# Performance work log

Hardware: AMD Instinct MI355X
Metric: run time of the kernel (lower is better)

Reference implementation:

```python
import jax, jax.numpy as jnp
import numpy as np

B, E, F = 16384, 128, 6
ITEM_V, CATE_V, HIST = 91718, 11, 50
I_IDX, J_IDX = np.triu_indices(F, k=1)  # 15 field pairs, loop order (0,1),(0,2),...
EPS = 1e-5


def _xavier(key, shape):
    fan_in, fan_out = shape[0], shape[-1]
    std = (2.0 / (fan_in + fan_out)) ** 0.5
    return std * jax.random.normal(key, shape, dtype=jnp.float32)


def setup_inputs() -> dict:
    key = jax.random.key(0)
    ks = jax.random.split(key, 20)
    inp = {
        'item_id': jax.random.randint(ks[0], (B,), 0, ITEM_V),
        'item_emb_d128': jax.random.normal(ks[1], (B, 128), dtype=jnp.float32),
        'likes_level': jax.random.randint(ks[2], (B,), 0, CATE_V),
        'views_level': jax.random.randint(ks[3], (B,), 0, CATE_V),
        'item_seq': jax.random.randint(ks[4], (B, HIST), 0, ITEM_V),
        # learned parameters
        'item_emb': 0.05 * jax.random.normal(ks[5], (ITEM_V, E), dtype=jnp.float32),
        'cate_emb': 0.05 * jax.random.normal(ks[6], (CATE_V, E), dtype=jnp.float32),
        'mm_W': _xavier(ks[7], (128, E)), 'mm_b': jnp.zeros((E,), jnp.float32),
        'ln_g': jnp.ones((E,), jnp.float32), 'ln_b': jnp.zeros((E,), jnp.float32),
        'se_W1': _xavier(ks[8], (F, F // 2)), 'se_b1': jnp.zeros((F // 2,), jnp.float32),
        'se_W2': _xavier(ks[9], (F // 2, F)), 'se_b2': jnp.zeros((F,), jnp.float32),
        'bi_W': _xavier(ks[10], (E, E)),
        'mlp_W1': _xavier(ks[11], (21 * E, 512)), 'mlp_b1': jnp.zeros((512,), jnp.float32),
        'bn1_g': jnp.ones((512,), jnp.float32), 'bn1_b': jnp.zeros((512,), jnp.float32),
        'bn1_rm': jnp.zeros((512,), jnp.float32), 'bn1_rv': jnp.ones((512,), jnp.float32),
        'mlp_W2': _xavier(ks[12], (512, 256)), 'mlp_b2': jnp.zeros((256,), jnp.float32),
        'bn2_g': jnp.ones((256,), jnp.float32), 'bn2_b': jnp.zeros((256,), jnp.float32),
        'bn2_rm': jnp.zeros((256,), jnp.float32), 'bn2_rv': jnp.ones((256,), jnp.float32),
        'mlp_W3': _xavier(ks[13], (256, 1)), 'mlp_b3': jnp.zeros((1,), jnp.float32),
    }
    return inp


def _forward(item_id, item_emb_d128, likes_level, views_level, item_seq,
             item_emb, cate_emb, mm_W, mm_b, ln_g, ln_b,
             se_W1, se_b1, se_W2, se_b2, bi_W,
             mlp_W1, mlp_b1, bn1_g, bn1_b, bn1_rm, bn1_rv,
             mlp_W2, mlp_b2, bn2_g, bn2_b, bn2_rm, bn2_rv,
             mlp_W3, mlp_b3):
    b = item_id.shape[0]
    tab = item_emb.at[0].set(0.0)  # padding_idx=0
    like_feat = cate_emb[likes_level]
    view_feat = cate_emb[views_level]
    item_feat = tab[item_id]
    # mm_proj: Linear -> LayerNorm -> ReLU
    mm = item_emb_d128 @ mm_W + mm_b
    mu = mm.mean(-1, keepdims=True)
    var = jnp.var(mm, axis=-1, keepdims=True)
    mm = jax.nn.relu((mm - mu) / jnp.sqrt(var + EPS) * ln_g + ln_b)
    # masked mean pooling over history
    seq_emb = tab[item_seq]                               # (B, HIST, E)
    valid = (item_seq != 0).astype(seq_emb.dtype)
    seq_sum = (seq_emb * valid[..., None]).sum(1)
    cnt = jnp.clip(valid.sum(1, keepdims=True), 1.0)
    hist_feat = seq_sum / cnt
    user_feat = jnp.zeros((b, E), seq_emb.dtype)
    x = jnp.stack([user_feat, like_feat, view_feat, item_feat, mm, hist_feat], axis=1)  # (B,6,E)
    # SENet
    z = x.mean(-1)
    w = jax.nn.sigmoid(jax.nn.relu(z @ se_W1 + se_b1) @ se_W2 + se_b2)
    xs = x * w[:, :, None]
    # bilinear 'all'
    xw = jnp.einsum('bfe,ed->bfd', xs, bi_W)
    p = xs[:, I_IDX, :] * xw[:, J_IDX, :]                 # (B,15,E)
    c = jnp.concatenate([xs.reshape(b, -1), p.reshape(b, -1)], axis=1)  # (B, 2688)
    # MLP head (eval mode: BN uses running stats, dropout off)
    h = c @ mlp_W1 + mlp_b1
    h = jax.nn.relu((h - bn1_rm) / jnp.sqrt(bn1_rv + EPS) * bn1_g + bn1_b)
    h = h @ mlp_W2 + mlp_b2
    h = jax.nn.relu((h - bn2_rm) / jnp.sqrt(bn2_rv + EPS) * bn2_g + bn2_b)
    logits = h @ mlp_W3 + mlp_b3
    return jax.nn.sigmoid(logits)[:, 0]


def reference(item_id, item_emb_d128, likes_level, views_level, item_seq,
              item_emb, cate_emb, mm_W, mm_b, ln_g, ln_b,
              se_W1, se_b1, se_W2, se_b2, bi_W,
              mlp_W1, mlp_b1, bn1_g, bn1_b, bn1_rm, bn1_rv,
              mlp_W2, mlp_b2, bn2_g, bn2_b, bn2_rm, bn2_rv,
              mlp_W3, mlp_b3):
    return _forward(item_id, item_emb_d128, likes_level, views_level, item_seq,
                    item_emb, cate_emb, mm_W, mm_b, ln_g, ln_b,
                    se_W1, se_b1, se_W2, se_b2, bi_W,
                    mlp_W1, mlp_b1, bn1_g, bn1_b, bn1_rm, bn1_rv,
                    mlp_W2, mlp_b2, bn2_g, bn2_b, bn2_rm, bn2_rv,
                    mlp_W3, mlp_b3)
```

## Files before the change

### kernel.cpp

```cpp
#include <hip/hip_runtime.h>
#include <hip/hip_bf16.h>

typedef __hip_bfloat16 bfloat;
typedef __bf16 bf16x8 __attribute__((ext_vector_type(8)));
typedef float f32x4 __attribute__((ext_vector_type(4)));

#define B_SZ   16384
#define E_DIM  128
#define HIST_L 50


#define IPACK 0x3221110000ULL
#define JPACK 0x3323213210ULL

__device__ __forceinline__ void gl_lds16(const void* g, void* l) {
    __builtin_amdgcn_global_load_lds(
        (const __attribute__((address_space(1))) unsigned int*)g,
        (__attribute__((address_space(3))) unsigned int*)l, 16, 0, 0);
}

__device__ __forceinline__ bf16x8 mul_bf16x8(bf16x8 a, bf16x8 b) {
    union { bf16x8 v; __hip_bfloat162 h[4]; } ua, ub, ur;
    ua.v = a; ub.v = b;
    #pragma unroll
    for (int i = 0; i < 4; ++i) ur.h[i] = __hmul2(ua.h[i], ub.h[i]);
    return ur.v;
}

template<int TB>
__global__ __launch_bounds__(256) void feat_kernel(
    const int* __restrict__ item_id,
    const int* __restrict__ likes, const int* __restrict__ views,
    const int* __restrict__ seq,
    const void* __restrict__ item_tab, const float* __restrict__ cate_emb,
    const float* __restrict__ mm,
    const float* __restrict__ ln_g, const float* __restrict__ ln_b,
    const float* __restrict__ se_W1, const float* __restrict__ se_b1,
    const float* __restrict__ se_W2, const float* __restrict__ se_b2,
    bfloat* __restrict__ xs)
{
    const int tid = threadIdx.x;
    const int r   = tid >> 7;
    const int e   = tid & 127;
    const int b   = blockIdx.x * 2 + r;
    const int w   = tid >> 6;

    __shared__ float redh[2][4][128];
    __shared__ int   seq_s[2][64];
    __shared__ float lnred[4], lnred2[4];
    __shared__ float zred[5][4];
    __shared__ float wsh[2][6];
    __shared__ int   cnt_s[2];

    if (e < 64) seq_s[r][e] = (e < HIST_L) ? seq[(size_t)b * HIST_L + e] : 0;
    __syncthreads();

    const int iid = item_id[b];
    const float like_v = cate_emb[likes[b] * 128 + e];
    const float view_v = cate_emb[views[b] * 128 + e];
    float item_v;
    if (TB) {
        const bfloat* tb = (const bfloat*)item_tab;
        item_v = __bfloat162float(tb[(size_t)iid * 128 + e]);
    } else {
        const float* tf = (const float*)item_tab;
        float raw = tf[(size_t)iid * 128 + e];
        item_v = iid ? raw : 0.f;
    }
    const float acc = mm[(size_t)b * 128 + e];

    const int q   = e >> 5;
    const int l32 = e & 31;
    float4 hs = make_float4(0.f, 0.f, 0.f, 0.f);
    if (TB) {
        const ushort* tb = (const ushort*)item_tab;
        #pragma unroll
        for (int g = 0; g < 13; ++g) {
            int s = seq_s[r][g * 4 + q];
            ushort4 v = *(const ushort4*)&tb[(size_t)s * 128 + l32 * 4];
            hs.x += __bfloat162float(__ushort_as_bfloat16(v.x));
            hs.y += __bfloat162float(__ushort_as_bfloat16(v.y));
            hs.z += __bfloat162float(__ushort_as_bfloat16(v.z));
            hs.w += __bfloat162float(__ushort_as_bfloat16(v.w));
        }
    } else {
        const float* tf = (const float*)item_tab;
        #pragma unroll
        for (int g = 0; g < 13; ++g) {
            int s = seq_s[r][g * 4 + q];
            const float4 v = *(const float4*)&tf[(size_t)s * 128 + l32 * 4];
            float m = (s != 0) ? 1.f : 0.f;
            hs.x = fmaf(v.x, m, hs.x);
            hs.y = fmaf(v.y, m, hs.y);
            hs.z = fmaf(v.z, m, hs.z);
            hs.w = fmaf(v.w, m, hs.w);
        }
    }

    {
        float v = acc;
        #pragma unroll
        for (int off = 32; off > 0; off >>= 1) v += __shfl_down(v, off, 64);
        if ((tid & 63) == 0) lnred[w] = v;
    }
    __syncthreads();
    const float mu = (lnred[2 * r] + lnred[2 * r + 1]) * (1.f / 128.f);
    const float d  = acc - mu;
    {
        float v = d * d;
        #pragma unroll
        for (int off = 32; off > 0; off >>= 1) v += __shfl_down(v, off, 64);
        if ((tid & 63) == 0) lnred2[w] = v;
    }
    redh[r][q][l32 * 4 + 0] = hs.x;
    redh[r][q][l32 * 4 + 1] = hs.y;
    redh[r][q][l32 * 4 + 2] = hs.z;
    redh[r][q][l32 * 4 + 3] = hs.w;
    if ((w & 1) == 0 && e < 64) {
        bool valid = (e < HIST_L) && (seq_s[r][e] != 0);
        unsigned long long m = __ballot(valid);
        if (e == 0) cnt_s[r] = (int)__popcll(m);
    }
    __syncthreads();
    const float var = (lnred2[2 * r] + lnred2[2 * r + 1]) * (1.f / 128.f);
    float xmm = d * rsqrtf(var + 1e-5f) * ln_g[e] + ln_b[e];
    xmm = fmaxf(xmm, 0.f);

    const int cnt = cnt_s[r] > 0 ? cnt_s[r] : 1;
    const float hist_v = (redh[r][0][e] + redh[r][1][e] +
                          redh[r][2][e] + redh[r][3][e]) / (float)cnt;

    {
        float s1 = like_v, s2 = view_v, s3 = item_v, s4 = xmm, s5 = hist_v;
        #pragma unroll
        for (int off = 32; off > 0; off >>= 1) {
            s1 += __shfl_down(s1, off, 64);
            s2 += __shfl_down(s2, off, 64);
            s3 += __shfl_down(s3, off, 64);
            s4 += __shfl_down(s4, off, 64);
            s5 += __shfl_down(s5, off, 64);
        }
        if ((tid & 63) == 0) {
            zred[0][w] = s1; zred[1][w] = s2; zred[2][w] = s3;
            zred[3][w] = s4; zred[4][w] = s5;
        }
    }
    __syncthreads();

    if (e == 0) {
        float z[6];
        z[0] = 0.f;
        #pragma unroll
        for (int f = 1; f < 6; ++f)
            z[f] = (zred[f - 1][2 * r] + zred[f - 1][2 * r + 1]) * (1.f / 128.f);
        float a[3];
        #pragma unroll
        for (int j = 0; j < 3; ++j) {
            float s = se_b1[j];
            #pragma unroll
            for (int f = 0; f < 6; ++f) s += z[f] * se_W1[f * 3 + j];
            a[j] = fmaxf(s, 0.f);
        }
        #pragma unroll
        for (int f = 0; f < 6; ++f) {
            float s = se_b2[f];
            #pragma unroll
            for (int j = 0; j < 3; ++j) s += a[j] * se_W2[j * 6 + f];
            wsh[r][f] = 1.f / (1.f + expf(-s));
        }
    }
    __syncthreads();

    bfloat* xrow = xs + (size_t)b * 640;
    xrow[0 * 128 + e] = __float2bfloat16(like_v * wsh[r][1]);
    xrow[1 * 128 + e] = __float2bfloat16(view_v * wsh[r][2]);
    xrow[2 * 128 + e] = __float2bfloat16(item_v * wsh[r][3]);
    xrow[3 * 128 + e] = __float2bfloat16(xmm    * wsh[r][4]);
    xrow[4 * 128 + e] = __float2bfloat16(hist_v * wsh[r][5]);
}

__global__ __launch_bounds__(256) void transpose_W1c(
    const float* __restrict__ W1, bfloat* __restrict__ W1t)
{
    int idx = blockIdx.x * 256 + threadIdx.x;
    if (idx < 512 * 1920) {
        int n = idx / 1920, kk = idx % 1920;
        int orig = kk + (kk < 640 ? 128 : 768);
        W1t[idx] = __float2bfloat16(W1[(size_t)orig * 512 + n]);
    }
}

__global__ __launch_bounds__(256) void prep_kernel(
    const float* __restrict__ W2, const float* __restrict__ bi_W,
    const float* __restrict__ mm_W,
    bfloat* __restrict__ W2t, bfloat* __restrict__ bWt,
    bfloat* __restrict__ mmWt,
    const float* __restrict__ lb1, const float* __restrict__ g1,
    const float* __restrict__ bb1, const float* __restrict__ rm1,
    const float* __restrict__ rv1,
    const float* __restrict__ lb2, const float* __restrict__ g2,
    const float* __restrict__ bb2, const float* __restrict__ rm2,
    const float* __restrict__ rv2,
    const float* __restrict__ mm_b,
    float* __restrict__ S1, float* __restrict__ T1,
    float* __restrict__ S2, float* __restrict__ T2,
    float* __restrict__ Tmm)
{
    int idx = blockIdx.x * 256 + threadIdx.x;
    if (idx < 131072) {
        int k = idx >> 8, n = idx & 255;
        W2t[(size_t)n * 512 + k] = __float2bfloat16(W2[idx]);
    } else if (idx < 147456) {
        int t = idx - 131072;
        int k = t >> 7, n = t & 127;
        bWt[n * 128 + k] = __float2bfloat16(bi_W[t]);
    } else if (idx < 163840) {
        int t = idx - 147456;
        int k = t >> 7, n = t & 127;
        mmWt[n * 128 + k] = __float2bfloat16(mm_W[t]);
    } else if (idx < 164352) {
        int j = idx - 163840;
        float s = g1[j] * rsqrtf(rv1[j] + 1e-5f);
        S1[j] = s;
        T1[j] = (lb1[j] - rm1[j]) * s + bb1[j];
    } else if (idx < 164608) {
        int j = idx - 164352;
        float s = g2[j] * rsqrtf(rv2[j] + 1e-5f);
        S2[j] = s;
        T2[j] = (lb2[j] - rm2[j]) * s + bb2[j];
    } else if (idx < 164736) {
        int j = idx - 164608;
        Tmm[j] = mm_b[j];
    }
}

__global__ __launch_bounds__(256) void cvt_emb(
    const float* __restrict__ in, bfloat* __restrict__ out, int n8)
{
    int idx = blockIdx.x * 256 + threadIdx.x;
    if (idx >= n8) return;
    if (idx < 16) {
        union { bf16x8 v; unsigned short s[8]; } z;
        #pragma unroll
        for (int i = 0; i < 8; ++i) z.s[i] = 0;
        ((bf16x8*)out)[idx] = z.v;
        return;
    }
    float4 f0 = ((const float4*)in)[idx * 2];
    float4 f1 = ((const float4*)in)[idx * 2 + 1];
    union { bf16x8 v; unsigned short s[8]; } u;
    u.s[0] = __bfloat16_as_ushort(__float2bfloat16(f0.x));
    u.s[1] = __bfloat16_as_ushort(__float2bfloat16(f0.y));
    u.s[2] = __bfloat16_as_ushort(__float2bfloat16(f0.z));
    u.s[3] = __bfloat16_as_ushort(__float2bfloat16(f0.w));
    u.s[4] = __bfloat16_as_ushort(__float2bfloat16(f1.x));
    u.s[5] = __bfloat16_as_ushort(__float2bfloat16(f1.y));
    u.s[6] = __bfloat16_as_ushort(__float2bfloat16(f1.z));
    u.s[7] = __bfloat16_as_ushort(__float2bfloat16(f1.w));
    ((bf16x8*)out)[idx] = u.v;
}

__global__ __launch_bounds__(256) void pair_kernel(
    const bfloat* __restrict__ xs, const bfloat* __restrict__ xw,
    bfloat* __restrict__ P, int total)
{
    int idx = blockIdx.x * 256 + threadIdx.x;
    if (idx >= total) return;
    int b = idx / 160, c = idx % 160;
    int pp = c >> 4, q = c & 15;
    int isl = (int)((IPACK >> (4 * pp)) & 15);
    int jsl = (int)((JPACK >> (4 * pp)) & 15);
    bf16x8 a = *(const bf16x8*)&xs[(size_t)b * 640 + isl * 128 + q * 8];
    bf16x8 w = *(const bf16x8*)&xw[((size_t)b * 4 + jsl) * 128 + q * 8];
    *(bf16x8*)&P[(size_t)b * 1280 + c * 8] = mul_bf16x8(a, w);
}

template<int MODE, int EPI, int F32OUT>
__global__ __launch_bounds__(256) void gemm_bt(
    const void* __restrict__ A, const bfloat* __restrict__ A2,
    const bfloat* __restrict__ Bt, void* __restrict__ C,
    int M, int N, int K,
    const float* __restrict__ S, const float* __restrict__ T)
{
    __shared__ __align__(16) short As[3][64 * 64];
    __shared__ __align__(16) short Bs[3][64 * 64];

    const int tid  = threadIdx.x;
    const int bm   = blockIdx.x * 64;
    const int bn   = blockIdx.y * 64;
    const int wave = tid >> 6;
    const int lane = tid & 63;
    const int wm   = (wave >> 1) * 32;
    const int wn   = (wave & 1) * 32;

    const short* Ag  = (const short*)A;
    const short* A2g = (const short*)A2;
    const short* Bg  = (const short*)Bt;

    f32x4 acc[2][2];
    #pragma unroll
    for (int i = 0; i < 2; ++i)
        #pragma unroll
        for (int j = 0; j < 2; ++j)
            acc[i][j] = (f32x4){0.f, 0.f, 0.f, 0.f};

    const int srow = tid >> 3;
    const int sck  = tid & 7;

    auto stage = [&](int buf, int kt) {
        #pragma unroll
        for (int rr = 0; rr < 2; ++rr) {
            int row = srow + rr * 32;
            int g   = sck ^ (row & 7);
            gl_lds16(&Bg[(long)(bn + row) * K + kt + g * 8],
                     &Bs[buf][row * 64 + sck * 8]);
        }
        if (MODE == 3) {
            const float* Af = (const float*)A;
            #pragma unroll
            for (int rr = 0; rr < 2; ++rr) {
                int row = srow + rr * 32;
                int g   = sck ^ (row & 7);
                long aoff = (long)(bm + row) * K + kt + g * 8;
                float4 f0 = *(const float4*)&Af[aoff];
                float4 f1 = *(const float4*)&Af[aoff + 4];
                union { bf16x8 v; unsigned short s[8]; } u;
                u.s[0] = __bfloat16_as_ushort(__float2bfloat16(f0.x));
                u.s[1] = __bfloat16_as_ushort(__float2bfloat16(f0.y));
                u.s[2] = __bfloat16_as_ushort(__float2bfloat16(f0.z));
                u.s[3] = __bfloat16_as_ushort(__float2bfloat16(f0.w));
                u.s[4] = __bfloat16_as_ushort(__float2bfloat16(f1.x));
                u.s[5] = __bfloat16_as_ushort(__float2bfloat16(f1.y));
                u.s[6] = __bfloat16_as_ushort(__float2bfloat16(f1.z));
                u.s[7] = __bfloat16_as_ushort(__float2bfloat16(f1.w));
                *(bf16x8*)&As[buf][row * 64 + sck * 8] = u.v;
            }
        } else {
            #pragma unroll
            for (int rr = 0; rr < 2; ++rr) {
                int row = srow + rr * 32;
                int g   = sck ^ (row & 7);
                const short* src;
                if (MODE == 4) {
                    long rb = (long)(bm + row);
                    src = (kt < 640)
                        ? &Ag [rb * 640  + kt + g * 8]
                        : &A2g[rb * 1280 + (kt - 640) + g * 8];
                } else if (MODE == 2) {
                    int gr = bm + row;
                    src = &Ag[((long)(gr >> 2)) * 640 +
                              ((gr & 3) + 1) * 128 + kt + g * 8];
                } else {
                    src = &Ag[(long)(bm + row) * K + kt + g * 8];
                }
                gl_lds16(src, &As[buf][row * 64 + sck * 8]);
            }
        }
    };

    const int rbase = lane & 15;
    const int cswz  = rbase & 7;

    const int nk = K >> 6;
    stage(0, 0);
    stage(1, 64);

    for (int i = 0; i < nk; ++i) {
        if (MODE == 3)
            asm volatile("s_waitcnt vmcnt(0) lgkmcnt(0)" ::: "memory");
        else if (i + 1 < nk)
            asm volatile("s_waitcnt vmcnt(4)" ::: "memory");
        else
            asm volatile("s_waitcnt vmcnt(0)" ::: "memory");
        __builtin_amdgcn_s_barrier();
        __builtin_amdgcn_sched_barrier(0);

        const int cur = i % 3;
        #pragma unroll
        for (int h = 0; h < 2; ++h) {
            const int cg = h * 4 + (lane >> 4);
            const int ca = (cg ^ cswz) << 3;
            bf16x8 af[2], bfr[2];
            #pragma unroll
            for (int mt = 0; mt < 2; ++mt)
                af[mt] = *(const bf16x8*)
                    &As[cur][(wm + mt * 16 + rbase) * 64 + ca];
            #pragma unroll
            for (int nt = 0; nt < 2; ++nt)
                bfr[nt] = *(const bf16x8*)
                    &Bs[cur][(wn + nt * 16 + rbase) * 64 + ca];
            #pragma unroll
            for (int mt = 0; mt < 2; ++mt)
                #pragma unroll
                for (int nt = 0; nt < 2; ++nt)
                    acc[mt][nt] = __builtin_amdgcn_mfma_f32_16x16x32_bf16(
                        af[mt], bfr[nt], acc[mt][nt], 0, 0, 0);
        }

        if (i + 2 < nk) stage((i + 2) % 3, (i + 2) << 6);
    }

    const int col0 = lane & 15;
    const int row0 = (lane >> 4) * 4;
    #pragma unroll
    for (int nt = 0; nt < 2; ++nt) {
        int col = bn + wn + nt * 16 + col0;
        float s = 1.f, t = 0.f;
        if (EPI) { s = (EPI == 1) ? S[col] : 1.f; t = T[col]; }
        #pragma unroll
        for (int mt = 0; mt < 2; ++mt) {
            #pragma unroll
            for (int i = 0; i < 4; ++i) {
                int row = bm + wm + mt * 16 + row0 + i;
                float v = acc[mt][nt][i];
                if (EPI == 1) v = fmaxf(v * s + t, 0.f);
                if (EPI == 2) v = v + t;
                if (F32OUT) ((float*)C)[(size_t)row * N + col] = v;
                else ((bfloat*)C)[(size_t)row * N + col] = __float2bfloat16(v);
            }
        }
    }
}

__global__ __launch_bounds__(256) void head_kernel(
    const bfloat* __restrict__ h2, const float* __restrict__ W3,
    const float* __restrict__ b3, float* __restrict__ out)
{
    int lane = threadIdx.x & 63;
    int row  = blockIdx.x * 4 + (threadIdx.x >> 6);
    float acc = 0.f;
    #pragma unroll
    for (int i = 0; i < 4; ++i)
        acc += __bfloat162float(h2[(size_t)row * 256 + i * 64 + lane]) *
               W3[i * 64 + lane];
    #pragma unroll
    for (int off = 32; off > 0; off >>= 1) acc += __shfl_down(acc, off, 64);
    if (lane == 0) {
        float l = acc + b3[0];
        out[row] = 1.f / (1.f + expf(-l));
    }
}

extern "C" void kernel_launch(void* const* d_in, const int* in_sizes, int n_in,
                              void* d_out, int out_size, void* d_ws, size_t ws_size,
                              hipStream_t stream) {
    const int*   item_id = (const int*)  d_in[0];
    const float* d128    = (const float*)d_in[1];
    const int*   likes   = (const int*)  d_in[2];
    const int*   views   = (const int*)  d_in[3];
    const int*   seq     = (const int*)  d_in[4];
    const float* item_emb= (const float*)d_in[5];
    const float* cate_emb= (const float*)d_in[6];
    const float* mm_W    = (const float*)d_in[7];
    const float* mm_b    = (const float*)d_in[8];
    const float* ln_g    = (const float*)d_in[9];
    const float* ln_b    = (const float*)d_in[10];
    const float* se_W1   = (const float*)d_in[11];
    const float* se_b1   = (const float*)d_in[12];
    const float* se_W2   = (const float*)d_in[13];
    const float* se_b2   = (const float*)d_in[14];
    const float* bi_W    = (const float*)d_in[15];
    const float* W1      = (const float*)d_in[16];
    const float* b1      = (const float*)d_in[17];
    const float* bn1_g   = (const float*)d_in[18];
    const float* bn1_b   = (const float*)d_in[19];
    const float* bn1_rm  = (const float*)d_in[20];
    const float* bn1_rv  = (const float*)d_in[21];
    const float* W2      = (const float*)d_in[22];
    const float* b2      = (const float*)d_in[23];
    const float* bn2_g   = (const float*)d_in[24];
    const float* bn2_b   = (const float*)d_in[25];
    const float* bn2_rm  = (const float*)d_in[26];
    const float* bn2_rv  = (const float*)d_in[27];
    const float* W3      = (const float*)d_in[28];
    const float* b3      = (const float*)d_in[29];

    const size_t fixed = 2300416;
    const size_t ITB   = 23479808;
    int CH; bool use_tb;
    if      (fixed + ITB + (size_t)16384 * 4864 <= ws_size) { CH = 16384; use_tb = true;  }
    else if (fixed + (size_t)16384 * 4864 <= ws_size)       { CH = 16384; use_tb = false; }
    else if (fixed + ITB + (size_t)8192 * 4864 <= ws_size)  { CH = 8192;  use_tb = true;  }
    else if (fixed + (size_t)8192 * 4864 <= ws_size)        { CH = 8192;  use_tb = false; }
    else if (fixed + ITB + (size_t)4096 * 4864 <= ws_size)  { CH = 4096;  use_tb = true;  }
    else if (fixed + (size_t)4096 * 4864 <= ws_size)        { CH = 4096;  use_tb = false; }
    else if (fixed + (size_t)2048 * 4864 <= ws_size)        { CH = 2048;  use_tb = false; }
    else                                                    { CH = 1024;  use_tb = false; }

    char* ws = (char*)d_ws;
    bfloat* W1t = (bfloat*)(ws);
    bfloat* W2t = (bfloat*)(ws + 1966080);
    bfloat* bWt = (bfloat*)(ws + 2228224);
    bfloat* mmWt= (bfloat*)(ws + 2260992);
    float*  S1  = (float*) (ws + 2293760);
    float*  T1  = (float*) (ws + 2295808);
    float*  S2  = (float*) (ws + 2297856);
    float*  T2  = (float*) (ws + 2298880);
    float*  Tmm = (float*) (ws + 2299904);
    bfloat* itemb = (bfloat*)(ws + fixed);
    char*   cb  = ws + fixed + (use_tb ? ITB : 0);
    bfloat* xs  = (bfloat*)(cb);
    bfloat* xw  = (bfloat*)(cb + (size_t)CH * 1280);
    bfloat* h1  = xw;
    bfloat* P   = (bfloat*)(cb + (size_t)CH * 2304);
    float*  mm  = (float*)P;
    bfloat* h2  = (bfloat*)P;

    transpose_W1c<<<(512 * 1920 + 255) / 256, 256, 0, stream>>>(W1, W1t);
    prep_kernel<<<(164736 + 255) / 256, 256, 0, stream>>>(
        W2, bi_W, mm_W, W2t, bWt, mmWt,
        b1, bn1_g, bn1_b, bn1_rm, bn1_rv,
        b2, bn2_g, bn2_b, bn2_rm, bn2_rv,
        mm_b, S1, T1, S2, T2, Tmm);
    if (use_tb) {
        const int n8 = 91718 * 128 / 8;
        cvt_emb<<<(n8 + 255) / 256, 256, 0, stream>>>(item_emb, itemb, n8);
    }

    for (int off = 0; off < B_SZ; off += CH) {
        dim3 gmm(CH / 64, 2);
        gemm_bt<3, 2, 1><<<gmm, 256, 0, stream>>>(
            d128 + (size_t)off * 128, nullptr, mmWt, mm,
            CH, 128, 128, nullptr, Tmm);

        if (use_tb)
            feat_kernel<1><<<CH / 2, 256, 0, stream>>>(
                item_id + off, likes + off, views + off,
                seq + (size_t)off * HIST_L, itemb, cate_emb, mm,
                ln_g, ln_b, se_W1, se_b1, se_W2, se_b2, xs);
        else
            feat_kernel<0><<<CH / 2, 256, 0, stream>>>(
                item_id + off, likes + off, views + off,
                seq + (size_t)off * HIST_L, item_emb, cate_emb, mm,
                ln_g, ln_b, se_W1, se_b1, se_W2, se_b2, xs);

        dim3 gxw(CH * 4 / 64, 2);
        gemm_bt<2, 0, 0><<<gxw, 256, 0, stream>>>(
            xs, nullptr, bWt, xw, CH * 4, 128, 128, nullptr, nullptr);

        pair_kernel<<<(CH * 160 + 255) / 256, 256, 0, stream>>>(
            xs, xw, P, CH * 160);

        dim3 g1(CH / 64, 8);
        gemm_bt<4, 1, 0><<<g1, 256, 0, stream>>>(
            xs, P, W1t, h1, CH, 512, 1920, S1, T1);

        dim3 g2(CH / 64, 4);
        gemm_bt<0, 1, 0><<<g2, 256, 0, stream>>>(
            h1, nullptr, W2t, h2, CH, 256, 512, S2, T2);

        head_kernel<<<CH / 4, 256, 0, stream>>>(h2, W3, b3, (float*)d_out + off);
    }
}
```

Baseline: 291.4 us.

## Enlarge GEMM tiles, fuse pairwise product into bilinear GEMM epilogue, tile W1 transpose

The generic bf16 MFMA GEMM moves from 64x64 tiles with K-step 64 to 128x128 tiles with K-step 32, giving each wave a 4x4 grid of 16x16 accumulators and setting launch bounds for 3 blocks per CU. The separate pair_kernel is removed: the xs@bi_W GEMM gains an epilogue that multiplies each output by the matching xs field slice and writes the pairwise products straight into P, so the xw intermediate no longer goes through memory. The W1 transpose now stages 64x64 tiles in shared memory for coalesced reads and writes. Larger tiles cut grid sizes sharply at small M per chunk, which may leave CUs idle, and the fused epilogue does scattered 2-byte stores.

```diff
diff --git a/kernel.cpp b/kernel.cpp
--- a/kernel.cpp
+++ b/kernel.cpp
@@ -10,21 +10,12 @@
 #define HIST_L 50
 
 
-#define IPACK 0x3221110000ULL
-#define JPACK 0x3323213210ULL
+__device__ __constant__ int ISL[10] = {0,0,0,0,1,1,1,2,2,3};
 
 __device__ __forceinline__ void gl_lds16(const void* g, void* l) {
     __builtin_amdgcn_global_load_lds(
         (const __attribute__((address_space(1))) unsigned int*)g,
         (__attribute__((address_space(3))) unsigned int*)l, 16, 0, 0);
-}
-
-__device__ __forceinline__ bf16x8 mul_bf16x8(bf16x8 a, bf16x8 b) {
-    union { bf16x8 v; __hip_bfloat162 h[4]; } ua, ub, ur;
-    ua.v = a; ub.v = b;
-    #pragma unroll
-    for (int i = 0; i < 4; ++i) ur.h[i] = __hmul2(ua.h[i], ub.h[i]);
-    return ur.v;
 }
 
 template<int TB>
@@ -182,11 +173,22 @@
 __global__ __launch_bounds__(256) void transpose_W1c(
     const float* __restrict__ W1, bfloat* __restrict__ W1t)
 {
-    int idx = blockIdx.x * 256 + threadIdx.x;
-    if (idx < 512 * 1920) {
-        int n = idx / 1920, kk = idx % 1920;
+    __shared__ float t[64][65];
+    const int tid = threadIdx.x;
+    const int kk0 = blockIdx.x * 64, n0 = blockIdx.y * 64;
+    const int j = tid & 63;
+    #pragma unroll
+    for (int p = 0; p < 16; ++p) {
+        int i = (tid >> 6) + p * 4;
+        int kk = kk0 + i;
         int orig = kk + (kk < 640 ? 128 : 768);
-        W1t[idx] = __float2bfloat16(W1[(size_t)orig * 512 + n]);
+        t[i][j] = W1[(size_t)orig * 512 + n0 + j];
+    }
+    __syncthreads();
+    #pragma unroll
+    for (int p = 0; p < 16; ++p) {
+        int i = (tid >> 6) + p * 4;
+        W1t[(size_t)(n0 + i) * 1920 + kk0 + j] = __float2bfloat16(t[j][i]);
     }
 }
 
@@ -260,67 +262,52 @@
     ((bf16x8*)out)[idx] = u.v;
 }
 
-__global__ __launch_bounds__(256) void pair_kernel(
-    const bfloat* __restrict__ xs, const bfloat* __restrict__ xw,
-    bfloat* __restrict__ P, int total)
-{
-    int idx = blockIdx.x * 256 + threadIdx.x;
-    if (idx >= total) return;
-    int b = idx / 160, c = idx % 160;
-    int pp = c >> 4, q = c & 15;
-    int isl = (int)((IPACK >> (4 * pp)) & 15);
-    int jsl = (int)((JPACK >> (4 * pp)) & 15);
-    bf16x8 a = *(const bf16x8*)&xs[(size_t)b * 640 + isl * 128 + q * 8];
-    bf16x8 w = *(const bf16x8*)&xw[((size_t)b * 4 + jsl) * 128 + q * 8];
-    *(bf16x8*)&P[(size_t)b * 1280 + c * 8] = mul_bf16x8(a, w);
-}
-
 template<int MODE, int EPI, int F32OUT>
-__global__ __launch_bounds__(256) void gemm_bt(
+__global__ __launch_bounds__(256, 3) void gemm_bt(
     const void* __restrict__ A, const bfloat* __restrict__ A2,
     const bfloat* __restrict__ Bt, void* __restrict__ C,
     int M, int N, int K,
     const float* __restrict__ S, const float* __restrict__ T)
 {
-    __shared__ __align__(16) short As[3][64 * 64];
-    __shared__ __align__(16) short Bs[3][64 * 64];
+    __shared__ __align__(16) short As[3][128 * 32];
+    __shared__ __align__(16) short Bs[3][128 * 32];
 
     const int tid  = threadIdx.x;
-    const int bm   = blockIdx.x * 64;
-    const int bn   = blockIdx.y * 64;
+    const int bm   = blockIdx.x * 128;
+    const int bn   = blockIdx.y * 128;
     const int wave = tid >> 6;
     const int lane = tid & 63;
-    const int wm   = (wave >> 1) * 32;
-    const int wn   = (wave & 1) * 32;
+    const int wm   = (wave >> 1) * 64;
+    const int wn   = (wave & 1) * 64;
 
     const short* Ag  = (const short*)A;
     const short* A2g = (const short*)A2;
     const short* Bg  = (const short*)Bt;
 
-    f32x4 acc[2][2];
+    f32x4 acc[4][4];
     #pragma unroll
-    for (int i = 0; i < 2; ++i)
-        #pragma unroll
-        for (int j = 0; j < 2; ++j)
+    for (int i = 0; i < 4; ++i)
+        #pragma unroll
+        for (int j = 0; j < 4; ++j)
             acc[i][j] = (f32x4){0.f, 0.f, 0.f, 0.f};
 
-    const int srow = tid >> 3;
-    const int sck  = tid & 7;
+    const int srow = tid >> 2;
+    const int sck  = tid & 3;
 
     auto stage = [&](int buf, int kt) {
         #pragma unroll
         for (int rr = 0; rr < 2; ++rr) {
-            int row = srow + rr * 32;
-            int g   = sck ^ (row & 7);
+            int row = srow + rr * 64;
+            int g   = sck ^ (row & 3);
             gl_lds16(&Bg[(long)(bn + row) * K + kt + g * 8],
-                     &Bs[buf][row * 64 + sck * 8]);
+                     &Bs[buf][row * 32 + sck * 8]);
         }
         if (MODE == 3) {
             const float* Af = (const float*)A;
             #pragma unroll
             for (int rr = 0; rr < 2; ++rr) {
-                int row = srow + rr * 32;
-                int g   = sck ^ (row & 7);
+                int row = srow + rr * 64;
+                int g   = sck ^ (row & 3);
                 long aoff = (long)(bm + row) * K + kt + g * 8;
                 float4 f0 = *(const float4*)&Af[aoff];
                 float4 f1 = *(const float4*)&Af[aoff + 4];
@@ -333,13 +320,13 @@
                 u.s[5] = __bfloat16_as_ushort(__float2bfloat16(f1.y));
                 u.s[6] = __bfloat16_as_ushort(__float2bfloat16(f1.z));
                 u.s[7] = __bfloat16_as_ushort(__float2bfloat16(f1.w));
-                *(bf16x8*)&As[buf][row * 64 + sck * 8] = u.v;
+                *(bf16x8*)&As[buf][row * 32 + sck * 8] = u.v;
             }
         } else {
             #pragma unroll
             for (int rr = 0; rr < 2; ++rr) {
-                int row = srow + rr * 32;
-                int g   = sck ^ (row & 7);
+                int row = srow + rr * 64;
+                int g   = sck ^ (row & 3);
                 const short* src;
                 if (MODE == 4) {
                     long rb = (long)(bm + row);
@@ -353,17 +340,18 @@
                 } else {
                     src = &Ag[(long)(bm + row) * K + kt + g * 8];
                 }
-                gl_lds16(src, &As[buf][row * 64 + sck * 8]);
+                gl_lds16(src, &As[buf][row * 32 + sck * 8]);
             }
         }
     };
 
     const int rbase = lane & 15;
-    const int cswz  = rbase & 7;
-
-    const int nk = K >> 6;
+    const int cg    = lane >> 4;
+    const int ca    = (cg ^ (rbase & 3)) << 3;
+
+    const int nk = K >> 5;
     stage(0, 0);
-    stage(1, 64);
+    stage(1, 32);
 
     for (int i = 0; i < nk; ++i) {
         if (MODE == 3)
@@ -376,47 +364,67 @@
         __builtin_amdgcn_sched_barrier(0);
 
         const int cur = i % 3;
-        #pragma unroll
-        for (int h = 0; h < 2; ++h) {
-            const int cg = h * 4 + (lane >> 4);
-            const int ca = (cg ^ cswz) << 3;
-            bf16x8 af[2], bfr[2];
+        bf16x8 af[4], bfr[4];
+        #pragma unroll
+        for (int mt = 0; mt < 4; ++mt)
+            af[mt] = *(const bf16x8*)
+                &As[cur][(wm + mt * 16 + rbase) * 32 + ca];
+        #pragma unroll
+        for (int nt = 0; nt < 4; ++nt)
+            bfr[nt] = *(const bf16x8*)
+                &Bs[cur][(wn + nt * 16 + rbase) * 32 + ca];
+        #pragma unroll
+        for (int mt = 0; mt < 4; ++mt)
             #pragma unroll
-            for (int mt = 0; mt < 2; ++mt)
-                af[mt] = *(const bf16x8*)
-                    &As[cur][(wm + mt * 16 + rbase) * 64 + ca];
-            #pragma unroll
-            for (int nt = 0; nt < 2; ++nt)
-                bfr[nt] = *(const bf16x8*)
-                    &Bs[cur][(wn + nt * 16 + rbase) * 64 + ca];
-            #pragma unroll
-            for (int mt = 0; mt < 2; ++mt)
-                #pragma unroll
-                for (int nt = 0; nt < 2; ++nt)
-                    acc[mt][nt] = __builtin_amdgcn_mfma_f32_16x16x32_bf16(
-                        af[mt], bfr[nt], acc[mt][nt], 0, 0, 0);
-        }
-
-        if (i + 2 < nk) stage((i + 2) % 3, (i + 2) << 6);
+            for (int nt = 0; nt < 4; ++nt)
+                acc[mt][nt] = __builtin_amdgcn_mfma_f32_16x16x32_bf16(
+                    af[mt], bfr[nt], acc[mt][nt], 0, 0, 0);
+
+        if (i + 2 < nk) stage((i + 2) % 3, (i + 2) << 5);
     }
 
     const int col0 = lane & 15;
     const int row0 = (lane >> 4) * 4;
     #pragma unroll
-    for (int nt = 0; nt < 2; ++nt) {
+    for (int nt = 0; nt < 4; ++nt) {
         int col = bn + wn + nt * 16 + col0;
         float s = 1.f, t = 0.f;
-        if (EPI) { s = (EPI == 1) ? S[col] : 1.f; t = T[col]; }
-        #pragma unroll
-        for (int mt = 0; mt < 2; ++mt) {
+        if (EPI == 1 || EPI == 2) { s = (EPI == 1) ? S[col] : 1.f; t = T[col]; }
+        #pragma unroll
+        for (int mt = 0; mt < 4; ++mt) {
             #pragma unroll
             for (int i = 0; i < 4; ++i) {
                 int row = bm + wm + mt * 16 + row0 + i;
                 float v = acc[mt][nt][i];
-                if (EPI == 1) v = fmaxf(v * s + t, 0.f);
-                if (EPI == 2) v = v + t;
-                if (F32OUT) ((float*)C)[(size_t)row * N + col] = v;
-                else ((bfloat*)C)[(size_t)row * N + col] = __float2bfloat16(v);
+                if (EPI == 3) {
+                    const bfloat* xsp = (const bfloat*)A;
+                    bfloat* Pp = (bfloat*)C;
+                    long b = row >> 2;
+                    const int npp  = (i == 0) ? 1 : (i == 1) ? 2 : (i == 2) ? 3 : 4;
+                    const int pp0s = (i == 0) ? 0 : (i == 1) ? 1 : (i == 2) ? 2 : 3;
+                    const int ppst = (i == 3) ? 0 : 0;
+                    (void)ppst;
+                    int pplist[4];
+                    if (i == 0) { pplist[0] = 0; }
+                    else if (i == 1) { pplist[0] = 1; pplist[1] = 4; }
+                    else if (i == 2) { pplist[0] = 2; pplist[1] = 5; pplist[2] = 7; }
+                    else { pplist[0] = 3; pplist[1] = 6; pplist[2] = 8; pplist[3] = 9; }
+                    (void)pp0s;
+                    #pragma unroll
+                    for (int t2 = 0; t2 < npp; ++t2) {
+                        int pp  = pplist[t2];
+                        int isl = ISL[pp];
+                        float xv = __bfloat162float(
+                            xsp[b * 640 + isl * 128 + col]);
+                        Pp[b * 1280 + pp * 128 + col] =
+                            __float2bfloat16(xv * v);
+                    }
+                } else {
+                    if (EPI == 1) v = fmaxf(v * s + t, 0.f);
+                    if (EPI == 2) v = v + t;
+                    if (F32OUT) ((float*)C)[(size_t)row * N + col] = v;
+                    else ((bfloat*)C)[(size_t)row * N + col] = __float2bfloat16(v);
+                }
             }
         }
     }
@@ -500,13 +508,12 @@
     bfloat* itemb = (bfloat*)(ws + fixed);
     char*   cb  = ws + fixed + (use_tb ? ITB : 0);
     bfloat* xs  = (bfloat*)(cb);
-    bfloat* xw  = (bfloat*)(cb + (size_t)CH * 1280);
-    bfloat* h1  = xw;
+    bfloat* h1  = (bfloat*)(cb + (size_t)CH * 1280);
     bfloat* P   = (bfloat*)(cb + (size_t)CH * 2304);
     float*  mm  = (float*)P;
     bfloat* h2  = (bfloat*)P;
 
-    transpose_W1c<<<(512 * 1920 + 255) / 256, 256, 0, stream>>>(W1, W1t);
+    transpose_W1c<<<dim3(30, 8), 256, 0, stream>>>(W1, W1t);
     prep_kernel<<<(164736 + 255) / 256, 256, 0, stream>>>(
         W2, bi_W, mm_W, W2t, bWt, mmWt,
         b1, bn1_g, bn1_b, bn1_rm, bn1_rv,
@@ -518,7 +525,7 @@
     }
 
     for (int off = 0; off < B_SZ; off += CH) {
-        dim3 gmm(CH / 64, 2);
+        dim3 gmm(CH / 128, 1);
         gemm_bt<3, 2, 1><<<gmm, 256, 0, stream>>>(
             d128 + (size_t)off * 128, nullptr, mmWt, mm,
             CH, 128, 128, nullptr, Tmm);
@@ -534,18 +541,15 @@
                 seq + (size_t)off * HIST_L, item_emb, cate_emb, mm,
                 ln_g, ln_b, se_W1, se_b1, se_W2, se_b2, xs);
 
-        dim3 gxw(CH * 4 / 64, 2);
-        gemm_bt<2, 0, 0><<<gxw, 256, 0, stream>>>(
-            xs, nullptr, bWt, xw, CH * 4, 128, 128, nullptr, nullptr);
-
-        pair_kernel<<<(CH * 160 + 255) / 256, 256, 0, stream>>>(
-            xs, xw, P, CH * 160);
-
-        dim3 g1(CH / 64, 8);
+        dim3 gxw(CH * 4 / 128, 1);
+        gemm_bt<2, 3, 0><<<gxw, 256, 0, stream>>>(
+            xs, nullptr, bWt, P, CH * 4, 128, 128, nullptr, nullptr);
+
+        dim3 g1(CH / 128, 4);
         gemm_bt<4, 1, 0><<<g1, 256, 0, stream>>>(
             xs, P, W1t, h1, CH, 512, 1920, S1, T1);
 
-        dim3 g2(CH / 64, 4);
+        dim3 g2(CH / 128, 2);
         gemm_bt<0, 1, 0><<<g2, 256, 0, stream>>>(
             h1, nullptr, W2t, h2, CH, 256, 512, S2, T2);
 
```

New measurement: 279.0 us. 4.3% less time.
